# Performance work log

Measured on AMD Instinct MI355X. Metric: run time of the kernel, lower is better.

Reference implementation:

```python
import jax, jax.numpy as jnp
import numpy as np

COMMITMENT_COST = 0.25


def _mlp(x, Ws, bs):
    # Linear layers with ReLU between hidden layers, linear output (rlpyt-style MlpModel).
    n = len(Ws)
    for i in range(n):
        x = x @ Ws[i] + bs[i]
        if i < n - 1:
            x = jax.nn.relu(x)
    return x


def setup_inputs() -> dict:
    key = jax.random.key(0)
    ks = jax.random.split(key, 16)
    B, D_in, H1, H2, D_code, K = 16384, 1024, 2048, 1024, 256, 1024

    def lin(kw, kb, fan_in, fan_out):
        lim = 1.0 / np.sqrt(fan_in)
        W = jax.random.uniform(kw, (fan_in, fan_out), jnp.float32, -lim, lim)
        b = jax.random.uniform(kb, (fan_out,), jnp.float32, -lim, lim)
        return W, b

    enc_W1, enc_b1 = lin(ks[0], ks[1], D_in, H1)
    enc_W2, enc_b2 = lin(ks[2], ks[3], H1, H2)
    enc_W3, enc_b3 = lin(ks[4], ks[5], H2, D_code)
    dec_W1, dec_b1 = lin(ks[6], ks[7], D_code, H2)
    dec_W2, dec_b2 = lin(ks[8], ks[9], H2, H1)
    dec_W3, dec_b3 = lin(ks[10], ks[11], H1, D_in)
    codebook = jax.random.uniform(ks[12], (K, D_code), jnp.float32, -1.0 / K, 1.0 / K)
    x = jax.random.normal(ks[13], (B, D_in), jnp.float32)
    return {
        "x": x,
        "enc_W1": enc_W1, "enc_b1": enc_b1,
        "enc_W2": enc_W2, "enc_b2": enc_b2,
        "enc_W3": enc_W3, "enc_b3": enc_b3,
        "codebook": codebook,
        "dec_W1": dec_W1, "dec_b1": dec_b1,
        "dec_W2": dec_W2, "dec_b2": dec_b2,
        "dec_W3": dec_W3, "dec_b3": dec_b3,
    }


def reference(x, enc_W1, enc_b1, enc_W2, enc_b2, enc_W3, enc_b3, codebook,
              dec_W1, dec_b1, dec_W2, dec_b2, dec_W3, dec_b3):
    # Encoder MLP -> z: [B, D_code]
    z = _mlp(x, [enc_W1, enc_W2, enc_W3], [enc_b1, enc_b2, enc_b3])
    # Squared L2 distances z vs codebook: [B, K]
    distances = (jnp.sum(z * z, axis=1, keepdims=True)
                 + jnp.sum(codebook * codebook, axis=1)
                 - 2.0 * jnp.einsum('bd,kd->bk', z, codebook))
    indices = jnp.argmin(distances, axis=1)  # [B]
    # one-hot scatter + matmul in the original == direct gather
    quantized = codebook[indices]            # [B, D_code]
    # training-mode losses
    e_latent_loss = jnp.mean((jax.lax.stop_gradient(quantized) - z) ** 2)
    q_latent_loss = jnp.mean((quantized - jax.lax.stop_gradient(z)) ** 2)
    loss = q_latent_loss + COMMITMENT_COST * e_latent_loss
    # straight-through estimator
    quantized_st = z + jax.lax.stop_gradient(quantized - z)
    reconstructed = _mlp(quantized_st, [dec_W1, dec_W2, dec_W3], [dec_b1, dec_b2, dec_b3])
    return reconstructed, quantized_st, loss, indices[:, None]
```

## Files before the change

kernel.cpp:

```cpp
#include <hip/hip_runtime.h>
#include <hip/hip_bf16.h>
#include <stdint.h>


#define BDIM  16384
#define DIN   1024
#define DH1   2048
#define DH2   1024
#define DCODE 256
#define KCODE 1024

typedef __hip_bfloat16 bf16;
typedef __attribute__((ext_vector_type(8))) short short8;
typedef __attribute__((ext_vector_type(4))) float f32x4;

__device__ __forceinline__ void gload16(const void* g, void* l)
{
    __builtin_amdgcn_global_load_lds(
        (const __attribute__((address_space(1))) unsigned int*)g,
        (__attribute__((address_space(3))) unsigned int*)l, 16, 0, 0);
}

__device__ __forceinline__ void swz_xcd(int gxlog, int* bx, int* by)
{
    unsigned wg = blockIdx.x;
    const unsigned nwg = gridDim.x;
    if ((nwg & 7u) == 0u) wg = (wg & 7u) * (nwg >> 3) + (wg >> 3);
    *bx = wg & ((1u << gxlog) - 1u);
    *by = wg >> gxlog;
}

__device__ __forceinline__ void split3(float f, ushort* h, ushort* m, ushort* l)
{
    bf16 bh = __float2bfloat16(f);
    float r1 = f - __bfloat162float(bh);
    bf16 bm = __float2bfloat16(r1);
    float r2 = r1 - __bfloat162float(bm);
    bf16 bl = __float2bfloat16(r2);
    *h = *(ushort*)&bh; *m = *(ushort*)&bm; *l = *(ushort*)&bl;
}

template<int RELU, int OUTK>
__global__ __launch_bounds__(512, 2)
void gemms(const ushort* __restrict__ Apl, const ushort* __restrict__ Bpl,
           const float* __restrict__ bias, void* __restrict__ C,
           void* __restrict__ C2,
           int M, int N, int K, size_t PA, size_t PB, size_t PC, int gxlog)
{
    __shared__ __align__(16) short As[3][3][128][32];
    __shared__ __align__(16) short Bs[3][3][128][32];
    const int tid  = threadIdx.x;
    const int lane = tid & 63;
    const int wave = tid >> 6;
    const int wm = (wave >> 1) << 5;
    const int wn = (wave & 1) << 6;
    const int fr = lane & 15, fq = lane >> 4;
    int bx, by;
    swz_xcd(gxlog, &bx, &by);
    const int row0 = by << 7, col0 = bx << 7;

    const int srow = (wave << 4) + (lane >> 2);
    const int sslot = lane & 3;
    const int skg = (sslot ^ ((srow >> 1) & 3)) << 3;

    const ushort* AgT = Apl + (size_t)(row0 + srow) * K + skg;
    const ushort* BgT = Bpl + (size_t)(col0 + srow) * K + skg;

    f32x4  acc[2][4];
    double dacc[2][4][4];
    #pragma unroll
    for (int i = 0; i < 2; ++i)
        #pragma unroll
        for (int j = 0; j < 4; ++j) {
            acc[i][j] = (f32x4)0.0f;
            #pragma unroll
            for (int r = 0; r < 4; ++r) dacc[i][j][r] = 0.0;
        }

    auto stage = [&](int b, int kb) {
        #pragma unroll
        for (int p = 0; p < 3; ++p) {
            gload16(AgT + (size_t)p * PA + kb, &As[b][p][wave << 4][0]);
            gload16(BgT + (size_t)p * PB + kb, &Bs[b][p][wave << 4][0]);
        }
    };

    stage(0, 0);
    stage(1, 32);
    const int nsteps = K >> 5;
    int b = 0, sb = 2;
    for (int s = 0; s < nsteps; ++s) {
        if (s + 2 < nsteps) {
            stage(sb, (s + 2) << 5);
            sb = (sb == 2) ? 0 : sb + 1;
            asm volatile("s_waitcnt vmcnt(12)" ::: "memory");
        } else if (s + 1 < nsteps) {
            asm volatile("s_waitcnt vmcnt(6)" ::: "memory");
        } else {
            asm volatile("s_waitcnt vmcnt(0)" ::: "memory");
        }
        __builtin_amdgcn_s_barrier();
        __builtin_amdgcn_sched_barrier(0);

        short8 bh[4], bm[4], bl[4];
        #pragma unroll
        for (int j = 0; j < 4; ++j) {
            const int bn = wn + (j << 4) + fr;
            const int bsl = (fq ^ ((bn >> 1) & 3)) << 3;
            bh[j] = *(const short8*)&Bs[b][0][bn][bsl];
            bm[j] = *(const short8*)&Bs[b][1][bn][bsl];
            bl[j] = *(const short8*)&Bs[b][2][bn][bsl];
        }
        #pragma unroll
        for (int i = 0; i < 2; ++i) {
            const int an = wm + (i << 4) + fr;
            const int asl = (fq ^ ((an >> 1) & 3)) << 3;
            short8 ah = *(const short8*)&As[b][0][an][asl];
            short8 am = *(const short8*)&As[b][1][an][asl];
            short8 al = *(const short8*)&As[b][2][an][asl];
            #pragma unroll
            for (int j = 0; j < 4; ++j) {
                acc[i][j] = __builtin_amdgcn_mfma_f32_16x16x32_bf16(ah, bh[j], acc[i][j], 0, 0, 0);
                acc[i][j] = __builtin_amdgcn_mfma_f32_16x16x32_bf16(ah, bm[j], acc[i][j], 0, 0, 0);
                acc[i][j] = __builtin_amdgcn_mfma_f32_16x16x32_bf16(am, bh[j], acc[i][j], 0, 0, 0);
                acc[i][j] = __builtin_amdgcn_mfma_f32_16x16x32_bf16(ah, bl[j], acc[i][j], 0, 0, 0);
                acc[i][j] = __builtin_amdgcn_mfma_f32_16x16x32_bf16(al, bh[j], acc[i][j], 0, 0, 0);
                acc[i][j] = __builtin_amdgcn_mfma_f32_16x16x32_bf16(am, bm[j], acc[i][j], 0, 0, 0);
            }
        }

        if (s & 1) {
            #pragma unroll
            for (int i = 0; i < 2; ++i)
                #pragma unroll
                for (int j = 0; j < 4; ++j) {
                    #pragma unroll
                    for (int r = 0; r < 4; ++r) dacc[i][j][r] += (double)acc[i][j][r];
                    acc[i][j] = (f32x4)0.0f;
                }
        }
        b = (b == 2) ? 0 : b + 1;
        __builtin_amdgcn_sched_barrier(0);
        __builtin_amdgcn_s_barrier();
    }
    #pragma unroll
    for (int i = 0; i < 2; ++i)
        #pragma unroll
        for (int j = 0; j < 4; ++j)
            #pragma unroll
            for (int r = 0; r < 4; ++r) dacc[i][j][r] += (double)acc[i][j][r];

    #pragma unroll
    for (int j = 0; j < 4; ++j) {
        const int n = col0 + wn + (j << 4) + fr;
        const double bv = (double)bias[n];
        #pragma unroll
        for (int i = 0; i < 2; ++i) {
            const int mb = row0 + wm + (i << 4) + (fq << 2);
            #pragma unroll
            for (int r = 0; r < 4; ++r) {
                double v = dacc[i][j][r] + bv;
                if (RELU) v = v > 0.0 ? v : 0.0;
                const size_t o = (size_t)(mb + r) * N + n;
                if (OUTK == 2 || OUTK == 3) ((double*)C)[o] = v;
                if (OUTK == 0 || OUTK == 3) {
                    ushort h, m, l;
                    split3((float)v, &h, &m, &l);
                    ushort* Cp = (ushort*)((OUTK == 0) ? C : C2);
                    Cp[o] = h; Cp[PC + o] = m; Cp[2 * PC + o] = l;
                }
            }
        }
    }
}

__global__ __launch_bounds__(512, 2)
void distm(const ushort* __restrict__ Zpl, const ushort* __restrict__ Cpl,
           const double* __restrict__ c2, double* __restrict__ psc,
           int* __restrict__ pix)
{
    __shared__ __align__(16) short As[3][128][40];
    __shared__ __align__(16) short Bs[3][128][40];
    const int tid  = threadIdx.x;
    const int lane = tid & 63;
    const int wave = tid >> 6;
    const int wm = (wave >> 1) << 5;
    const int wn = (wave & 1) << 6;
    const int fr = lane & 15, fq = lane >> 4;
    int bx, by;
    swz_xcd(3, &bx, &by);
    const int row0 = by << 7, col0 = bx << 7;
    const int sr = tid >> 2, sc = (tid & 3) << 3;
    const size_t PZ = (size_t)BDIM * DCODE;
    const size_t PC = (size_t)KCODE * DCODE;

    const ushort* Ag = Zpl + (size_t)(row0 + sr) * DCODE + sc;
    const ushort* Bg = Cpl + (size_t)(col0 + sr) * DCODE + sc;

    f32x4  acc[2][4];
    double dacc[2][4][4];
    #pragma unroll
    for (int i = 0; i < 2; ++i)
        #pragma unroll
        for (int j = 0; j < 4; ++j) {
            acc[i][j] = (f32x4)0.0f;
            #pragma unroll
            for (int r = 0; r < 4; ++r) dacc[i][j][r] = 0.0;
        }

    short8 sa[3], sb[3];
    #pragma unroll
    for (int p = 0; p < 3; ++p) {
        sa[p] = *(const short8*)(Ag + (size_t)p * PZ);
        sb[p] = *(const short8*)(Bg + (size_t)p * PC);
    }

    const int nsteps = DCODE >> 5;
    for (int s = 0; s < nsteps; ++s) {
        __syncthreads();
        #pragma unroll
        for (int p = 0; p < 3; ++p) {
            *(short8*)&As[p][sr][sc] = sa[p];
            *(short8*)&Bs[p][sr][sc] = sb[p];
        }
        __syncthreads();
        if (s + 1 < nsteps) {
            const int kb = (s + 1) << 5;
            #pragma unroll
            for (int p = 0; p < 3; ++p) {
                sa[p] = *(const short8*)(Ag + (size_t)p * PZ + kb);
                sb[p] = *(const short8*)(Bg + (size_t)p * PC + kb);
            }
        }

        short8 bh[4], bm[4], bl[4];
        #pragma unroll
        for (int j = 0; j < 4; ++j) {
            const int bn = wn + (j << 4) + fr;
            bh[j] = *(const short8*)&Bs[0][bn][fq << 3];
            bm[j] = *(const short8*)&Bs[1][bn][fq << 3];
            bl[j] = *(const short8*)&Bs[2][bn][fq << 3];
        }
        #pragma unroll
        for (int i = 0; i < 2; ++i) {
            const int an = wm + (i << 4) + fr;
            short8 ah = *(const short8*)&As[0][an][fq << 3];
            short8 am = *(const short8*)&As[1][an][fq << 3];
            short8 al = *(const short8*)&As[2][an][fq << 3];
            #pragma unroll
            for (int j = 0; j < 4; ++j) {
                acc[i][j] = __builtin_amdgcn_mfma_f32_16x16x32_bf16(ah, bh[j], acc[i][j], 0, 0, 0);
                acc[i][j] = __builtin_amdgcn_mfma_f32_16x16x32_bf16(ah, bm[j], acc[i][j], 0, 0, 0);
                acc[i][j] = __builtin_amdgcn_mfma_f32_16x16x32_bf16(am, bh[j], acc[i][j], 0, 0, 0);
                acc[i][j] = __builtin_amdgcn_mfma_f32_16x16x32_bf16(ah, bl[j], acc[i][j], 0, 0, 0);
                acc[i][j] = __builtin_amdgcn_mfma_f32_16x16x32_bf16(al, bh[j], acc[i][j], 0, 0, 0);
                acc[i][j] = __builtin_amdgcn_mfma_f32_16x16x32_bf16(am, bm[j], acc[i][j], 0, 0, 0);
            }
        }

        if (s & 1) {
            #pragma unroll
            for (int i = 0; i < 2; ++i)
                #pragma unroll
                for (int j = 0; j < 4; ++j) {
                    #pragma unroll
                    for (int r = 0; r < 4; ++r) dacc[i][j][r] += (double)acc[i][j][r];
                    acc[i][j] = (f32x4)0.0f;
                }
        }
    }
    #pragma unroll
    for (int i = 0; i < 2; ++i)
        #pragma unroll
        for (int j = 0; j < 4; ++j)
            #pragma unroll
            for (int r = 0; r < 4; ++r) dacc[i][j][r] += (double)acc[i][j][r];

    __syncthreads();
    double* scb = (double*)&As[0][0][0];
    int*    sib = (int*)(scb + 256);

    #pragma unroll
    for (int i = 0; i < 2; ++i) {
        #pragma unroll
        for (int r = 0; r < 4; ++r) {
            double bs = 1e300; int bi = 0;
            #pragma unroll
            for (int j = 0; j < 4; ++j) {
                const int n = col0 + wn + (j << 4) + fr;
                const double s = c2[n] - 2.0 * dacc[i][j][r];
                if (s < bs) { bs = s; bi = n; }
            }
            #pragma unroll
            for (int msk = 1; msk < 16; msk <<= 1) {
                double os = __shfl_xor(bs, msk, 64);
                int    oi = __shfl_xor(bi, msk, 64);
                if (os < bs || (os == bs && oi < bi)) { bs = os; bi = oi; }
            }
            if (fr == 0) {
                const int lr = wm + (i << 4) + (fq << 2) + r;
                scb[lr * 2 + (wave & 1)] = bs;
                sib[lr * 2 + (wave & 1)] = bi;
            }
        }
    }
    __syncthreads();
    if (tid < 128) {
        double s0 = scb[tid * 2], s1 = scb[tid * 2 + 1];
        int    i0 = sib[tid * 2], i1 = sib[tid * 2 + 1];
        const bool t1 = (s1 < s0) || (s1 == s0 && i1 < i0);
        const size_t o = (size_t)(row0 + tid) * (KCODE / 128) + bx;
        psc[o] = t1 ? s1 : s0;
        pix[o] = t1 ? i1 : i0;
    }
}

__global__ __launch_bounds__(256)
void reduce8(const double* __restrict__ psc, const int* __restrict__ pix,
             int* __restrict__ idx_out)
{
    const int row = blockIdx.x * 256 + threadIdx.x;
    const double* ps = psc + (size_t)row * (KCODE / 128);
    const int*    pi = pix + (size_t)row * (KCODE / 128);
    double m = ps[0]; int mi = pi[0];
    #pragma unroll
    for (int t = 1; t < KCODE / 128; ++t) {
        double s = ps[t]; int c = pi[t];
        if (s < m || (s == m && c < mi)) { m = s; mi = c; }
    }
    idx_out[row] = mi;
}

template<int RELU, int OUTBF>
__global__ __launch_bounds__(256)
void gemmb2(const ushort* __restrict__ A, const ushort* __restrict__ Bt,
            const float* __restrict__ bias, void* __restrict__ C,
            int M, int N, int K, int gxlog)
{
    __shared__ __align__(16) short As[3][128][32];
    __shared__ __align__(16) short Bs[3][128][32];
    const int tid  = threadIdx.x;
    const int lane = tid & 63;
    const int wave = tid >> 6;
    const int wm = (wave >> 1) << 6, wn = (wave & 1) << 6;
    const int fr = lane & 15;
    const int fq = lane >> 4;
    int bx, by;
    swz_xcd(gxlog, &bx, &by);
    const int row0 = by << 7, col0 = bx << 7;

    const int sr0 = (wave << 5) + (lane >> 2);
    const int sslot = lane & 3;
    const int kg0 = (sslot ^ ((sr0 >> 1) & 3)) << 3;
    const int sr1 = sr0 + 16;
    const int kg1 = (sslot ^ ((sr1 >> 1) & 3)) << 3;

    const ushort* Ag0 = A  + (size_t)(row0 + sr0) * K + kg0;
    const ushort* Ag1 = A  + (size_t)(row0 + sr1) * K + kg1;
    const ushort* Bg0 = Bt + (size_t)(col0 + sr0) * K + kg0;
    const ushort* Bg1 = Bt + (size_t)(col0 + sr1) * K + kg1;

    f32x4 acc[4][4];
    #pragma unroll
    for (int i = 0; i < 4; ++i)
        #pragma unroll
        for (int j = 0; j < 4; ++j) acc[i][j] = (f32x4)0.0f;

    auto stage = [&](int b, int kb) {
        gload16(Ag0 + kb, &As[b][wave << 5][0]);
        gload16(Ag1 + kb, &As[b][(wave << 5) + 16][0]);
        gload16(Bg0 + kb, &Bs[b][wave << 5][0]);
        gload16(Bg1 + kb, &Bs[b][(wave << 5) + 16][0]);
    };

    stage(0, 0);
    stage(1, 32);
    const int nsteps = K >> 5;
    int b = 0, sbuf = 2;
    for (int s = 0; s < nsteps; ++s) {
        if (s + 2 < nsteps) {
            stage(sbuf, (s + 2) << 5);
            sbuf = (sbuf == 2) ? 0 : sbuf + 1;
            asm volatile("s_waitcnt vmcnt(8)" ::: "memory");
        } else if (s + 1 < nsteps) {
            asm volatile("s_waitcnt vmcnt(4)" ::: "memory");
        } else {
            asm volatile("s_waitcnt vmcnt(0)" ::: "memory");
        }
        __builtin_amdgcn_s_barrier();
        __builtin_amdgcn_sched_barrier(0);

        short8 af[4], bf[4];
        #pragma unroll
        for (int i = 0; i < 4; ++i) {
            const int an = wm + (i << 4) + fr;
            af[i] = *(const short8*)&As[b][an][(fq ^ ((an >> 1) & 3)) << 3];
        }
        #pragma unroll
        for (int j = 0; j < 4; ++j) {
            const int bn = wn + (j << 4) + fr;
            bf[j] = *(const short8*)&Bs[b][bn][(fq ^ ((bn >> 1) & 3)) << 3];
        }
        #pragma unroll
        for (int i = 0; i < 4; ++i)
            #pragma unroll
            for (int j = 0; j < 4; ++j)
                acc[i][j] = __builtin_amdgcn_mfma_f32_16x16x32_bf16(
                                af[i], bf[j], acc[i][j], 0, 0, 0);

        b = (b == 2) ? 0 : b + 1;
        __builtin_amdgcn_sched_barrier(0);
        __builtin_amdgcn_s_barrier();
    }

    #pragma unroll
    for (int j = 0; j < 4; ++j) {
        const int n = col0 + wn + (j << 4) + fr;
        const float bv = bias[n];
        #pragma unroll
        for (int i = 0; i < 4; ++i) {
            const int mb = row0 + wm + (i << 4) + (fq << 2);
            #pragma unroll
            for (int r = 0; r < 4; ++r) {
                float v = acc[i][j][r] + bv;
                if (RELU) v = fmaxf(v, 0.0f);
                size_t o = (size_t)(mb + r) * N + n;
                if (OUTBF) ((bf16*)C)[o]  = __float2bfloat16(v);
                else       ((float*)C)[o] = v;
            }
        }
    }
}

__global__ __launch_bounds__(256)
void wtrans(const float* __restrict__ W, ushort* __restrict__ Wt, int K, int N)
{
    __shared__ float tile[64][65];
    const int tid = threadIdx.x;
    const int kb = blockIdx.y << 6, nb = blockIdx.x << 6;
    const int r = tid >> 4, c4 = (tid & 15) << 2;
    #pragma unroll
    for (int s = 0; s < 4; ++s) {
        float4 v = *(const float4*)(W + (size_t)(kb + r + (s << 4)) * N + nb + c4);
        tile[r + (s << 4)][c4 + 0] = v.x; tile[r + (s << 4)][c4 + 1] = v.y;
        tile[r + (s << 4)][c4 + 2] = v.z; tile[r + (s << 4)][c4 + 3] = v.w;
    }
    __syncthreads();
    #pragma unroll
    for (int s = 0; s < 4; ++s) {
        const int n = r + (s << 4);
        ushort u[4];
        #pragma unroll
        for (int l = 0; l < 4; ++l) {
            bf16 h = __float2bfloat16(tile[c4 + l][n]);
            u[l] = *(ushort*)&h;
        }
        *(ushort4*)(Wt + (size_t)(nb + n) * K + kb + c4) = make_ushort4(u[0], u[1], u[2], u[3]);
    }
}

__global__ __launch_bounds__(256)
void wsplit(const float* __restrict__ W, ushort* __restrict__ Wt, int K, int N)
{
    __shared__ float tile[64][65];
    const int tid = threadIdx.x;
    const int kb = blockIdx.y << 6, nb = blockIdx.x << 6;
    const int r = tid >> 4, c4 = (tid & 15) << 2;
    const size_t NK = (size_t)N * K;
    #pragma unroll
    for (int s = 0; s < 4; ++s) {
        float4 v = *(const float4*)(W + (size_t)(kb + r + (s << 4)) * N + nb + c4);
        tile[r + (s << 4)][c4 + 0] = v.x; tile[r + (s << 4)][c4 + 1] = v.y;
        tile[r + (s << 4)][c4 + 2] = v.z; tile[r + (s << 4)][c4 + 3] = v.w;
    }
    __syncthreads();
    #pragma unroll
    for (int s = 0; s < 4; ++s) {
        const int n = r + (s << 4);
        ushort h[4], m[4], l[4];
        #pragma unroll
        for (int e = 0; e < 4; ++e) split3(tile[c4 + e][n], &h[e], &m[e], &l[e]);
        const size_t o = (size_t)(nb + n) * K + kb + c4;
        *(ushort4*)(Wt + o)          = make_ushort4(h[0], h[1], h[2], h[3]);
        *(ushort4*)(Wt + NK + o)     = make_ushort4(m[0], m[1], m[2], m[3]);
        *(ushort4*)(Wt + 2 * NK + o) = make_ushort4(l[0], l[1], l[2], l[3]);
    }
}

__global__ __launch_bounds__(256)
void xsplit(const float* __restrict__ X, ushort* __restrict__ Xp, size_t P)
{
    const size_t i = ((size_t)blockIdx.x * 256 + threadIdx.x) << 2;
    float4 v = *(const float4*)(X + i);
    ushort h[4], m[4], l[4];
    split3(v.x, &h[0], &m[0], &l[0]);
    split3(v.y, &h[1], &m[1], &l[1]);
    split3(v.z, &h[2], &m[2], &l[2]);
    split3(v.w, &h[3], &m[3], &l[3]);
    *(ushort4*)(Xp + i)         = make_ushort4(h[0], h[1], h[2], h[3]);
    *(ushort4*)(Xp + P + i)     = make_ushort4(m[0], m[1], m[2], m[3]);
    *(ushort4*)(Xp + 2 * P + i) = make_ushort4(l[0], l[1], l[2], l[3]);
}

__global__ __launch_bounds__(64)
void c2_k(const float* __restrict__ cb, double* __restrict__ c2)
{
    int code = blockIdx.x, l = threadIdx.x;
    float4 v = *(const float4*)(cb + (size_t)code * DCODE + (l << 2));
    double s = (double)v.x * v.x + (double)v.y * v.y
             + (double)v.z * v.z + (double)v.w * v.w;
    #pragma unroll
    for (int off = 32; off; off >>= 1) s += __shfl_down(s, off, 64);
    if (l == 0) c2[code] = s;
}

__global__ __launch_bounds__(256)
void gather_k(const int* __restrict__ idx_in, const float* __restrict__ cb,
              const double* __restrict__ z, ushort* __restrict__ qstb,
              float* __restrict__ out_qst, float* __restrict__ out_idx,
              double* __restrict__ psum)
{
    const int tid  = threadIdx.x;
    const int row  = (blockIdx.x << 2) + (tid >> 6);
    const int lane = tid & 63;
    const int d    = lane << 2;
    const int idx  = idx_in[row];

    float4 qv = *(const float4*)(cb + (size_t)idx * DCODE + d);
    const double* zp = z + (size_t)row * DCODE + d;
    double2 z0 = *(const double2*)(zp);
    double2 z1 = *(const double2*)(zp + 2);

    double q[4] = {(double)qv.x, (double)qv.y, (double)qv.z, (double)qv.w};
    double zz[4] = {z0.x, z0.y, z1.x, z1.y};
    double qs[4];
    double s = 0.0;
    #pragma unroll
    for (int e = 0; e < 4; ++e) {
        double diff = q[e] - zz[e];
        qs[e] = zz[e] + diff;
        s += diff * diff;
    }
    *(float4*)(out_qst + (size_t)row * DCODE + d) =
        make_float4((float)qs[0], (float)qs[1], (float)qs[2], (float)qs[3]);
    ushort u[4];
    #pragma unroll
    for (int e = 0; e < 4; ++e) {
        bf16 h = __float2bfloat16((float)qs[e]);
        u[e] = *(ushort*)&h;
    }
    *(ushort4*)(qstb + (size_t)row * DCODE + d) = make_ushort4(u[0], u[1], u[2], u[3]);

    #pragma unroll
    for (int off = 32; off; off >>= 1) s += __shfl_down(s, off, 64);
    __shared__ double sred[4];
    if (lane == 0) {
        sred[tid >> 6] = s;
        out_idx[row] = (float)idx;
    }
    __syncthreads();
    if (tid == 0) psum[blockIdx.x] = sred[0] + sred[1] + sred[2] + sred[3];
}

__global__ __launch_bounds__(256)
void loss_k(const double* __restrict__ psum, float* __restrict__ out_loss)
{
    const int tid = threadIdx.x;
    double s = 0.0;
    for (int i = tid; i < BDIM / 4; i += 256) s += psum[i];
    #pragma unroll
    for (int off = 32; off; off >>= 1) s += __shfl_down(s, off, 64);
    __shared__ double sred[4];
    if ((tid & 63) == 0) sred[tid >> 6] = s;
    __syncthreads();
    if (tid == 0)
        out_loss[0] = (float)(1.25 * (sred[0] + sred[1] + sred[2] + sred[3]) / 4194304.0);
}

extern "C" void kernel_launch(void* const* d_in, const int* in_sizes, int n_in,
                              void* d_out, int out_size, void* d_ws, size_t ws_size,
                              hipStream_t stream)
{
    const float* x   = (const float*)d_in[0];
    const float* eW1 = (const float*)d_in[1];
    const float* eb1 = (const float*)d_in[2];
    const float* eW2 = (const float*)d_in[3];
    const float* eb2 = (const float*)d_in[4];
    const float* eW3 = (const float*)d_in[5];
    const float* eb3 = (const float*)d_in[6];
    const float* cbk = (const float*)d_in[7];
    const float* dW1 = (const float*)d_in[8];
    const float* db1 = (const float*)d_in[9];
    const float* dW2 = (const float*)d_in[10];
    const float* db2 = (const float*)d_in[11];
    const float* dW3 = (const float*)d_in[12];
    const float* db3 = (const float*)d_in[13];

    const size_t EPS1 = (size_t)3 * 2048 * 1024 * 2;
    const size_t EPS2 = (size_t)3 * 1024 * 2048 * 2;
    const size_t EPS3 = (size_t)3 * 256 * 1024 * 2;
    const size_t EPS  = EPS1 + EPS2 + EPS3;
    const size_t FIX_W1 = (size_t)1024 * 256 * 2;
    const size_t FIX_W2 = (size_t)2048 * 1024 * 2;
    const size_t FIX_W3 = (size_t)1024 * 2048 * 2;
    const size_t ZB   = (size_t)BDIM * DCODE * 8;
    const size_t ZPLB = (size_t)3 * BDIM * DCODE * 2;
    const size_t QSTB = (size_t)BDIM * DCODE * 2;
    const size_t IDXB = (size_t)BDIM * 4;
    const size_t NPT  = KCODE / 128;
    const size_t PSCB = (size_t)BDIM * NPT * 8;
    const size_t PIXB = (size_t)BDIM * NPT * 4;
    const size_t CBPB = (size_t)3 * KCODE * DCODE * 2;
    const size_t PSUM = (size_t)(BDIM / 4) * 8;

    const size_t PERSIST = FIX_W1 + FIX_W2 + FIX_W3 + ZB + ZPLB + QSTB + IDXB
                         + PSCB + PIXB + CBPB + PSUM + 8192 + 256;

    int R = BDIM;
    while (R > 256 && PERSIST + EPS + (size_t)R * 24576 > ws_size) R >>= 1;
    const int nch = BDIM / R;

    char* ws = (char*)d_ws;
    size_t off = 0;
    ushort* eP1  = (ushort*)(ws + off); off += EPS1;
    ushort* eP2  = (ushort*)(ws + off); off += EPS2;
    ushort* eP3  = (ushort*)(ws + off); off += EPS3;
    ushort* xpl  = (ushort*)(ws + off); off += (size_t)R * 6144;
    ushort* h1pl = (ushort*)(ws + off); off += (size_t)R * 12288;
    ushort* h2pl = (ushort*)(ws + off); off += (size_t)R * 6144;
    ushort* dh1b = xpl;
    ushort* dh2b = h1pl;
    ushort* Wt1  = (ushort*)(ws + off); off += FIX_W1;
    ushort* Wt2  = (ushort*)(ws + off); off += FIX_W2;
    ushort* Wt3  = (ushort*)(ws + off); off += FIX_W3;
    double* zb   = (double*)(ws + off); off += ZB;
    ushort* zpl  = (ushort*)(ws + off); off += ZPLB;
    ushort* qstb = (ushort*)(ws + off); off += QSTB;
    int*    idxb = (int*)(ws + off);    off += IDXB;
    double* psc  = (double*)(ws + off); off += PSCB;
    int*    pix  = (int*)(ws + off);    off += PIXB;
    ushort* cbP  = (ushort*)(ws + off); off += CBPB;
    double* psum = (double*)(ws + off); off += PSUM;
    double* c2   = (double*)(ws + off); off += 8192;

    float* out      = (float*)d_out;
    float* out_rec  = out;
    float* out_qst  = out + (size_t)BDIM * DIN;
    float* out_loss = out_qst + (size_t)BDIM * DCODE;
    float* out_idx  = out_loss + 1;

    c2_k<<<KCODE, 64, 0, stream>>>(cbk, c2);
    wtrans<<<dim3(1024 / 64,  256 / 64), 256, 0, stream>>>(dW1, Wt1,  256, 1024);
    wtrans<<<dim3(2048 / 64, 1024 / 64), 256, 0, stream>>>(dW2, Wt2, 1024, 2048);
    wtrans<<<dim3(1024 / 64, 2048 / 64), 256, 0, stream>>>(dW3, Wt3, 2048, 1024);
    wsplit<<<dim3(2048 / 64, 1024 / 64), 256, 0, stream>>>(eW1, eP1, 1024, 2048);
    wsplit<<<dim3(1024 / 64, 2048 / 64), 256, 0, stream>>>(eW2, eP2, 2048, 1024);
    wsplit<<<dim3( 256 / 64, 1024 / 64), 256, 0, stream>>>(eW3, eP3, 1024,  256);
    xsplit<<<(KCODE * DCODE) / 1024, 256, 0, stream>>>(cbk, cbP, (size_t)KCODE * DCODE);

    const int rb = R / 128;

    for (int c = 0; c < nch; ++c) {
        const float* xc = x + (size_t)c * R * DIN;
        double* zb_c  = zb + (size_t)c * R * DCODE;
        ushort* zpl_c = zpl + (size_t)c * R * DCODE;
        xsplit<<<R, 256, 0, stream>>>(xc, xpl, (size_t)R * DIN);
        gemms<1, 0><<<16 * rb, 512, 0, stream>>>(
            xpl, eP1, eb1, h1pl, nullptr, R, DH1, DIN,
            (size_t)R * DIN, (size_t)DH1 * DIN, (size_t)R * DH1, 4);
        gemms<1, 0><<<8 * rb, 512, 0, stream>>>(
            h1pl, eP2, eb2, h2pl, nullptr, R, DH2, DH1,
            (size_t)R * DH1, (size_t)DH2 * DH1, (size_t)R * DH2, 3);
        gemms<0, 3><<<2 * rb, 512, 0, stream>>>(
            h2pl, eP3, eb3, zb_c, zpl_c, R, DCODE, DH2,
            (size_t)R * DH2, (size_t)DCODE * DH2, (size_t)BDIM * DCODE, 1);
    }

    distm<<<8 * (BDIM / 128), 512, 0, stream>>>(zpl, cbP, c2, psc, pix);
    reduce8<<<BDIM / 256, 256, 0, stream>>>(psc, pix, idxb);

    gather_k<<<BDIM / 4, 256, 0, stream>>>(idxb, cbk, zb, qstb, out_qst, out_idx, psum);

    for (int c = 0; c < nch; ++c) {
        const ushort* qst_c = qstb + (size_t)c * R * DCODE;
        float* rec_c = out_rec + (size_t)c * R * DIN;
        gemmb2<1, 1><<<8 * rb, 256, 0, stream>>>(qst_c, Wt1, db1, dh1b, R, DH2, DCODE, 3);
        gemmb2<1, 1><<<16 * rb, 256, 0, stream>>>(dh1b, Wt2, db2, dh2b, R, DH1, DH2, 4);
        gemmb2<0, 0><<<8 * rb, 256, 0, stream>>>(dh2b, Wt3, db3, rec_c, R, DIN, DH1, 3);
    }

    loss_k<<<1, 256, 0, stream>>>(psum, out_loss);
}
```

Baseline: 1.550 ms.

## Shrink split-precision encoder GEMM tile to 64x128 with 256 threads and double buffering

The 3-plane bf16-split encoder GEMM moves from 512-thread blocks on 128x128 tiles with triple-buffered LDS to 256-thread blocks on 64x128 tiles with double-buffered LDS. The main loop is unrolled by two and s_setprio is raised around the MFMA section. The aim is to cut LDS use per block so more blocks stay resident, and to launch twice as many blocks for better occupancy and latency hiding. The cost is less reuse of the B tile per block, since each B tile is now loaded for only 64 rows, plus a shallower prefetch pipeline.

Result: faster. 1.436 ms (-7.4%).

```diff
diff --git a/kernel.cpp b/kernel.cpp
--- a/kernel.cpp
+++ b/kernel.cpp
@@ -41,14 +41,14 @@
 }
 
 template<int RELU, int OUTK>
-__global__ __launch_bounds__(512, 2)
+__global__ __launch_bounds__(256, 2)
 void gemms(const ushort* __restrict__ Apl, const ushort* __restrict__ Bpl,
            const float* __restrict__ bias, void* __restrict__ C,
            void* __restrict__ C2,
            int M, int N, int K, size_t PA, size_t PB, size_t PC, int gxlog)
 {
-    __shared__ __align__(16) short As[3][3][128][32];
-    __shared__ __align__(16) short Bs[3][3][128][32];
+    __shared__ __align__(16) short As[2][3][64][32];
+    __shared__ __align__(16) short Bs[2][3][128][32];
     const int tid  = threadIdx.x;
     const int lane = tid & 63;
     const int wave = tid >> 6;
@@ -57,14 +57,20 @@
     const int fr = lane & 15, fq = lane >> 4;
     int bx, by;
     swz_xcd(gxlog, &bx, &by);
-    const int row0 = by << 7, col0 = bx << 7;
-
-    const int srow = (wave << 4) + (lane >> 2);
+    const int row0 = by << 6, col0 = bx << 7;
+
+    const int sr16  = lane >> 2;
     const int sslot = lane & 3;
-    const int skg = (sslot ^ ((srow >> 1) & 3)) << 3;
-
-    const ushort* AgT = Apl + (size_t)(row0 + srow) * K + skg;
-    const ushort* BgT = Bpl + (size_t)(col0 + srow) * K + skg;
+    const int arow  = (wave << 4) + sr16;
+    const int brow0 = (wave << 5) + sr16;
+    const int brow1 = brow0 + 16;
+    const int akg  = (sslot ^ ((arow  >> 1) & 3)) << 3;
+    const int bkg0 = (sslot ^ ((brow0 >> 1) & 3)) << 3;
+    const int bkg1 = (sslot ^ ((brow1 >> 1) & 3)) << 3;
+
+    const ushort* AgT = Apl + (size_t)(row0 + arow)  * K + akg;
+    const ushort* Bg0 = Bpl + (size_t)(col0 + brow0) * K + bkg0;
+    const ushort* Bg1 = Bpl + (size_t)(col0 + brow1) * K + bkg1;
 
     f32x4  acc[2][4];
     double dacc[2][4][4];
@@ -81,27 +87,12 @@
         #pragma unroll
         for (int p = 0; p < 3; ++p) {
             gload16(AgT + (size_t)p * PA + kb, &As[b][p][wave << 4][0]);
-            gload16(BgT + (size_t)p * PB + kb, &Bs[b][p][wave << 4][0]);
+            gload16(Bg0 + (size_t)p * PB + kb, &Bs[b][p][wave << 5][0]);
+            gload16(Bg1 + (size_t)p * PB + kb, &Bs[b][p][(wave << 5) + 16][0]);
         }
     };
 
-    stage(0, 0);
-    stage(1, 32);
-    const int nsteps = K >> 5;
-    int b = 0, sb = 2;
-    for (int s = 0; s < nsteps; ++s) {
-        if (s + 2 < nsteps) {
-            stage(sb, (s + 2) << 5);
-            sb = (sb == 2) ? 0 : sb + 1;
-            asm volatile("s_waitcnt vmcnt(12)" ::: "memory");
-        } else if (s + 1 < nsteps) {
-            asm volatile("s_waitcnt vmcnt(6)" ::: "memory");
-        } else {
-            asm volatile("s_waitcnt vmcnt(0)" ::: "memory");
-        }
-        __builtin_amdgcn_s_barrier();
-        __builtin_amdgcn_sched_barrier(0);
-
+    auto compute = [&](int b) {
         short8 bh[4], bm[4], bl[4];
         #pragma unroll
         for (int j = 0; j < 4; ++j) {
@@ -111,6 +102,7 @@
             bm[j] = *(const short8*)&Bs[b][1][bn][bsl];
             bl[j] = *(const short8*)&Bs[b][2][bn][bsl];
         }
+        __builtin_amdgcn_s_setprio(1);
         #pragma unroll
         for (int i = 0; i < 2; ++i) {
             const int an = wm + (i << 4) + fr;
@@ -128,27 +120,39 @@
                 acc[i][j] = __builtin_amdgcn_mfma_f32_16x16x32_bf16(am, bm[j], acc[i][j], 0, 0, 0);
             }
         }
-
-        if (s & 1) {
-            #pragma unroll
-            for (int i = 0; i < 2; ++i)
-                #pragma unroll
-                for (int j = 0; j < 4; ++j) {
-                    #pragma unroll
-                    for (int r = 0; r < 4; ++r) dacc[i][j][r] += (double)acc[i][j][r];
-                    acc[i][j] = (f32x4)0.0f;
-                }
-        }
-        b = (b == 2) ? 0 : b + 1;
+        __builtin_amdgcn_s_setprio(0);
+    };
+
+    stage(0, 0);
+    const int nsteps = K >> 5;
+    for (int s = 0; s < nsteps; s += 2) {
+        stage(1, (s + 1) << 5);
+        asm volatile("s_waitcnt vmcnt(9)" ::: "memory");
+        __builtin_amdgcn_s_barrier();
+        __builtin_amdgcn_sched_barrier(0);
+        compute(0);
         __builtin_amdgcn_sched_barrier(0);
         __builtin_amdgcn_s_barrier();
-    }
-    #pragma unroll
-    for (int i = 0; i < 2; ++i)
-        #pragma unroll
-        for (int j = 0; j < 4; ++j)
-            #pragma unroll
-            for (int r = 0; r < 4; ++r) dacc[i][j][r] += (double)acc[i][j][r];
+        if (s + 2 < nsteps) {
+            stage(0, (s + 2) << 5);
+            asm volatile("s_waitcnt vmcnt(9)" ::: "memory");
+        } else {
+            asm volatile("s_waitcnt vmcnt(0)" ::: "memory");
+        }
+        __builtin_amdgcn_s_barrier();
+        __builtin_amdgcn_sched_barrier(0);
+        compute(1);
+        #pragma unroll
+        for (int i = 0; i < 2; ++i)
+            #pragma unroll
+            for (int j = 0; j < 4; ++j) {
+                #pragma unroll
+                for (int r = 0; r < 4; ++r) dacc[i][j][r] += (double)acc[i][j][r];
+                acc[i][j] = (f32x4)0.0f;
+            }
+        __builtin_amdgcn_sched_barrier(0);
+        __builtin_amdgcn_s_barrier();
+    }
 
     #pragma unroll
     for (int j = 0; j < 4; ++j) {
@@ -658,20 +662,21 @@
     wsplit<<<dim3( 256 / 64, 1024 / 64), 256, 0, stream>>>(eW3, eP3, 1024,  256);
     xsplit<<<(KCODE * DCODE) / 1024, 256, 0, stream>>>(cbk, cbP, (size_t)KCODE * DCODE);
 
-    const int rb = R / 128;
+    const int rb64 = R / 64;
+    const int rb   = R / 128;
 
     for (int c = 0; c < nch; ++c) {
         const float* xc = x + (size_t)c * R * DIN;
         double* zb_c  = zb + (size_t)c * R * DCODE;
         ushort* zpl_c = zpl + (size_t)c * R * DCODE;
         xsplit<<<R, 256, 0, stream>>>(xc, xpl, (size_t)R * DIN);
-        gemms<1, 0><<<16 * rb, 512, 0, stream>>>(
+        gemms<1, 0><<<16 * rb64, 256, 0, stream>>>(
             xpl, eP1, eb1, h1pl, nullptr, R, DH1, DIN,
             (size_t)R * DIN, (size_t)DH1 * DIN, (size_t)R * DH1, 4);
-        gemms<1, 0><<<8 * rb, 512, 0, stream>>>(
+        gemms<1, 0><<<8 * rb64, 256, 0, stream>>>(
             h1pl, eP2, eb2, h2pl, nullptr, R, DH2, DH1,
             (size_t)R * DH1, (size_t)DH2 * DH1, (size_t)R * DH2, 3);
-        gemms<0, 3><<<2 * rb, 512, 0, stream>>>(
+        gemms<0, 3><<<2 * rb64, 256, 0, stream>>>(
             h2pl, eP3, eb3, zb_c, zpl_c, R, DCODE, DH2,
             (size_t)R * DH2, (size_t)DCODE * DH2, (size_t)BDIM * DCODE, 1);
     }
```
